# Kernel tuning notes

Measured on AMD Instinct MI355X. Metric: run time of the kernel, lower is better.

Reference implementation:

```python
import jax, jax.numpy as jnp
import numpy as np

B, T, D, H = 64, 512, 512, 512


def _gru_direction(x, w_ih, w_hh, b_ih, b_hh, reverse):
    # x: (B,T,D); w_ih: (3H,D); w_hh: (3H,H); biases: (3H,)
    # Precompute input projections for all timesteps (same math as per-step W_ih @ x_t).
    zi_all = jnp.einsum('btd,gd->btg', x, w_ih) + b_ih  # (B,T,3H)
    if reverse:
        zi_all = zi_all[:, ::-1]
    h0 = jnp.zeros((B, H), x.dtype)

    def step(h, zi):
        zh = h @ w_hh.T + b_hh                      # (B,3H), includes b_hh inside r-gated term
        r = jax.nn.sigmoid(zi[:, :H] + zh[:, :H])
        z = jax.nn.sigmoid(zi[:, H:2 * H] + zh[:, H:2 * H])
        n = jnp.tanh(zi[:, 2 * H:] + r * zh[:, 2 * H:])
        h_new = (1 - z) * n + z * h
        return h_new, h_new

    h_last, outs = jax.lax.scan(step, h0, jnp.swapaxes(zi_all, 0, 1))  # outs: (T,B,H)
    outs = jnp.swapaxes(outs, 0, 1)  # (B,T,H)
    if reverse:
        outs = outs[:, ::-1]
    return outs, h_last


def setup_inputs() -> dict:
    key = jax.random.key(0)
    ks = jax.random.split(key, 9)
    K = 1.0 / np.sqrt(H)

    def u(k, shape):
        return jax.random.uniform(k, shape, jnp.float32, -K, K)

    return {
        'x': jax.random.normal(ks[0], (B, T, D), jnp.float32),
        'w_ih_fw': u(ks[1], (3 * H, D)),
        'w_hh_fw': u(ks[2], (3 * H, H)),
        'b_ih_fw': u(ks[3], (3 * H,)),
        'b_hh_fw': u(ks[4], (3 * H,)),
        'w_ih_bw': u(ks[5], (3 * H, D)),
        'w_hh_bw': u(ks[6], (3 * H, H)),
        'b_ih_bw': u(ks[7], (3 * H,)),
        'b_hh_bw': u(ks[8], (3 * H,)),
    }


def reference(x, w_ih_fw, w_hh_fw, b_ih_fw, b_hh_fw, w_ih_bw, w_hh_bw, b_ih_bw, b_hh_bw):
    out_fw, h_fw = _gru_direction(x, w_ih_fw, w_hh_fw, b_ih_fw, b_hh_fw, reverse=False)
    out_bw, h_bw = _gru_direction(x, w_ih_bw, w_hh_bw, b_ih_bw, b_hh_bw, reverse=True)
    outputs = jnp.concatenate([out_fw, out_bw], axis=2)  # (B,T,2H)
    return outputs, h_fw, h_bw
```

## Files before the change

### kernel.cpp

```cpp
#include <hip/hip_runtime.h>
#include <hip/hip_bf16.h>

typedef __bf16 bf16_t;
typedef bf16_t bf16x8 __attribute__((ext_vector_type(8)));
typedef float  f32x4  __attribute__((ext_vector_type(4)));

constexpr int Bb = 64;
constexpr int T  = 512;
constexpr int D  = 512;
constexpr int H  = 512;
constexpr int M1 = Bb * T;
constexpr int N1 = 3 * H;

#define LDK 72

template <typename ZT>
__global__ __launch_bounds__(256) void zi_gemm(
    const float* __restrict__ x,
    const float* __restrict__ w_fw, const float* __restrict__ w_bw,
    const float* __restrict__ b_fw, const float* __restrict__ b_bw,
    ZT* __restrict__ zi)
{
    const int dir = blockIdx.z;
    const float* __restrict__ w    = dir ? w_bw : w_fw;
    const float* __restrict__ bias = dir ? b_bw : b_fw;
    ZT* __restrict__ out = zi + (size_t)dir * M1 * N1;

    const int m0 = blockIdx.x * 128;
    const int n0 = blockIdx.y * 128;

    __shared__ bf16_t As[128 * LDK];
    __shared__ bf16_t Bs[128 * LDK];

    const int tid  = threadIdx.x;
    const int lane = tid & 63;
    const int wave = tid >> 6;
    const int wm = (wave >> 1) * 64;
    const int wn = (wave & 1) * 64;
    const int q   = lane >> 4;
    const int l16 = lane & 15;

    f32x4 acc[4][4] = {};

    for (int kt = 0; kt < D; kt += 64) {
#pragma unroll
        for (int p = 0; p < 4; ++p) {
            int idx = tid + p * 256;
            int row = idx >> 3;
            int seg = idx & 7;
            const float* sa = &x[(size_t)(m0 + row) * D + kt + seg * 8];
            const float* sb = &w[(size_t)(n0 + row) * D + kt + seg * 8];
            float4 a0 = *(const float4*)sa;
            float4 a1 = *(const float4*)(sa + 4);
            float4 b0 = *(const float4*)sb;
            float4 b1 = *(const float4*)(sb + 4);
            bf16x8 ta = { (bf16_t)a0.x, (bf16_t)a0.y, (bf16_t)a0.z, (bf16_t)a0.w,
                          (bf16_t)a1.x, (bf16_t)a1.y, (bf16_t)a1.z, (bf16_t)a1.w };
            bf16x8 tb = { (bf16_t)b0.x, (bf16_t)b0.y, (bf16_t)b0.z, (bf16_t)b0.w,
                          (bf16_t)b1.x, (bf16_t)b1.y, (bf16_t)b1.z, (bf16_t)b1.w };
            *(bf16x8*)&As[row * LDK + seg * 8] = ta;
            *(bf16x8*)&Bs[row * LDK + seg * 8] = tb;
        }
        __syncthreads();
#pragma unroll
        for (int kk = 0; kk < 64; kk += 32) {
            bf16x8 afr[4], bfr[4];
#pragma unroll
            for (int i = 0; i < 4; ++i)
                afr[i] = *(const bf16x8*)&As[(wm + i * 16 + l16) * LDK + kk + q * 8];
#pragma unroll
            for (int j = 0; j < 4; ++j)
                bfr[j] = *(const bf16x8*)&Bs[(wn + j * 16 + l16) * LDK + kk + q * 8];
#pragma unroll
            for (int i = 0; i < 4; ++i)
#pragma unroll
                for (int j = 0; j < 4; ++j)
                    acc[i][j] = __builtin_amdgcn_mfma_f32_16x16x32_bf16(
                        afr[i], bfr[j], acc[i][j], 0, 0, 0);
        }
        __syncthreads();
    }

#pragma unroll
    for (int i = 0; i < 4; ++i) {
        int grow = m0 + wm + i * 16 + q * 4;
#pragma unroll
        for (int j = 0; j < 4; ++j) {
            int gcol = n0 + wn + j * 16 + l16;
            float bia = bias[gcol];
#pragma unroll
            for (int r = 0; r < 4; ++r) {
                float v = acc[i][j][r] + bia;
                out[(size_t)(grow + r) * N1 + gcol] = (ZT)v;
            }
        }
    }
}

template <typename ZT>
__device__ __forceinline__ float zcvt(unsigned v)
{
    if constexpr (sizeof(ZT) == 4)
        return __builtin_bit_cast(float, v);
    else
        return __builtin_bit_cast(float, v << 16);
}

template <typename ZT>
__global__ __launch_bounds__(256, 1) void gru_persist(
    const ZT* __restrict__ zi,
    const float* __restrict__ whh_fw,
    const float* __restrict__ whh_bw,
    const float* __restrict__ bhh_fw,
    const float* __restrict__ bhh_bw,
    bf16_t* __restrict__ hb16,
    float* __restrict__ out,
    float* __restrict__ hlast,
    unsigned int* __restrict__ bar)
{
    const int dir = blockIdx.y;
    const float* __restrict__ whh = dir ? whh_bw : whh_fw;
    const float* __restrict__ bhh = dir ? bhh_bw : bhh_fw;
    const ZT* __restrict__ zid = zi + (size_t)dir * M1 * N1;
    unsigned int* cnt = bar + dir * 32;

    const int tid  = threadIdx.x;
    const int lane = tid & 63;
    const int wave = tid >> 6;
    const int q    = lane >> 4;
    const int l16  = lane & 15;
    const int c0   = blockIdx.x * 16;
    const int wm   = wave * 16;
    const int c    = c0 + l16;

    bf16x8 wreg[3][16];
#pragma unroll
    for (int g = 0; g < 3; ++g) {
        const float* wr = &whh[(size_t)(g * H + c0 + l16) * H];
#pragma unroll
        for (int kt = 0; kt < 16; ++kt) {
            float4 a = *(const float4*)&wr[kt * 32 + q * 8];
            float4 b = *(const float4*)&wr[kt * 32 + q * 8 + 4];
            wreg[g][kt] = (bf16x8){ (bf16_t)a.x, (bf16_t)a.y, (bf16_t)a.z, (bf16_t)a.w,
                                    (bf16_t)b.x, (bf16_t)b.y, (bf16_t)b.z, (bf16_t)b.w };
        }
    }
    const float bh_r = bhh[c];
    const float bh_z = bhh[H + c];
    const float bh_n = bhh[2 * H + c];

    bf16_t* hbase16 = hb16 + (size_t)dir * 2 * Bb * H;
    const bf16_t* rd0 = hbase16 + (size_t)(wm + l16) * H + q * 8;
    const bf16_t* rd1 = rd0 + Bb * H;
    bf16_t* wr0 = hbase16 + (size_t)(wm + q * 4) * H + c;
    bf16_t* wr1 = wr0 + Bb * H;

    float hcur[4] = {0.f, 0.f, 0.f, 0.f};

    unsigned zr[3][4];

#define ISSUE_ZI(tt) do {                                                         \
    _Pragma("unroll")                                                             \
    for (int r_ = 0; r_ < 4; ++r_) {                                              \
        const ZT* zb_ = zid + ((size_t)(wm + q * 4 + r_) * T + (size_t)(tt)) * N1 \
                            + H + c;                                              \
        if constexpr (sizeof(ZT) == 4) {                                          \
            asm volatile("global_load_dword %0, %1, off offset:-2048"             \
                         : "=&v"(zr[0][r_]) : "v"(zb_) : "memory");               \
            asm volatile("global_load_dword %0, %1, off"                          \
                         : "=&v"(zr[1][r_]) : "v"(zb_) : "memory");               \
            asm volatile("global_load_dword %0, %1, off offset:2048"              \
                         : "=&v"(zr[2][r_]) : "v"(zb_) : "memory");               \
        } else {                                                                  \
            asm volatile("global_load_ushort %0, %1, off offset:-1024"            \
                         : "=&v"(zr[0][r_]) : "v"(zb_) : "memory");               \
            asm volatile("global_load_ushort %0, %1, off"                         \
                         : "=&v"(zr[1][r_]) : "v"(zb_) : "memory");               \
            asm volatile("global_load_ushort %0, %1, off offset:1024"             \
                         : "=&v"(zr[2][r_]) : "v"(zb_) : "memory");               \
        }                                                                         \
    }                                                                             \
} while (0)

    {
        const int t0 = dir ? (T - 1) : 0;
        ISSUE_ZI(t0);
    }

#pragma unroll 1
    for (int s = 0; s < T; ++s) {
        const int t = dir ? (T - 1 - s) : s;
        const bf16_t* hrd = (s & 1) ? rd1 : rd0;
        bf16_t*       hwr = (s & 1) ? wr0 : wr1;

        bf16x8 hf[16];
#define LDH(i, OFFSTR)                                                        \
        asm volatile("global_load_dwordx4 %0, %1, off offset:" OFFSTR         \
                     " sc0 sc1" : "=&v"(hf[i]) : "v"(hrd) : "memory");
        LDH(0,  "0")    LDH(1,  "64")   LDH(2,  "128")  LDH(3,  "192")
        LDH(4,  "256")  LDH(5,  "320")  LDH(6,  "384")  LDH(7,  "448")
        LDH(8,  "512")  LDH(9,  "576")  LDH(10, "640")  LDH(11, "704")
        LDH(12, "768")  LDH(13, "832")  LDH(14, "896")  LDH(15, "960")
#undef LDH
        __builtin_amdgcn_sched_barrier(0);
        asm volatile("s_waitcnt vmcnt(0)" ::: "memory");
        __builtin_amdgcn_sched_barrier(0);

        f32x4 acc[3][2] = {};
#pragma unroll
        for (int kt = 0; kt < 16; ++kt) {
#pragma unroll
            for (int g = 0; g < 3; ++g)
                acc[g][kt & 1] = __builtin_amdgcn_mfma_f32_16x16x32_bf16(
                    hf[kt], wreg[g][kt], acc[g][kt & 1], 0, 0, 0);
        }

        float hn4[4];
#pragma unroll
        for (int r = 0; r < 4; ++r) {
            float zh_r = acc[0][0][r] + acc[0][1][r] + bh_r;
            float zh_z = acc[1][0][r] + acc[1][1][r] + bh_z;
            float zh_n = acc[2][0][r] + acc[2][1][r] + bh_n;
            float zi_r = zcvt<ZT>(zr[0][r]);
            float zi_z = zcvt<ZT>(zr[1][r]);
            float zi_n = zcvt<ZT>(zr[2][r]);
            float rg = 1.f / (1.f + __expf(-(zi_r + zh_r)));
            float zg = 1.f / (1.f + __expf(-(zi_z + zh_z)));
            float ng = tanhf(zi_n + rg * zh_n);
            float hn = (1.f - zg) * ng + zg * hcur[r];
            hcur[r] = hn;
            hn4[r] = hn;
        }

        __builtin_amdgcn_sched_barrier(0);
#pragma unroll
        for (int r = 0; r < 4; ++r) {
            const int row = wm + q * 4 + r;
            unsigned short hs = __builtin_bit_cast(unsigned short, (bf16_t)hn4[r]);
            asm volatile("global_store_short %0, %1, off sc0 sc1"
                         :: "v"(hwr + (size_t)r * H), "v"(hs) : "memory");
            float* optr = out + ((size_t)row * T + t) * (2 * H) + (size_t)dir * H + c;
            asm volatile("global_store_dword %0, %1, off"
                         :: "v"(optr), "v"(hn4[r]) : "memory");
        }
        __builtin_amdgcn_sched_barrier(0);

        if (s < T - 1) {
            const int tn = dir ? (T - 2 - s) : (s + 1);
            ISSUE_ZI(tn);
            __builtin_amdgcn_sched_barrier(0);
            asm volatile("s_waitcnt vmcnt(12)" ::: "memory");
            __builtin_amdgcn_sched_barrier(0);
            __syncthreads();
            if (tid == 0) {
                __hip_atomic_fetch_add(cnt, 1u, __ATOMIC_RELAXED,
                                       __HIP_MEMORY_SCOPE_AGENT);
                const unsigned target = 32u * (unsigned)(s + 1);
                unsigned tries = 0;
                while (__hip_atomic_load(cnt, __ATOMIC_RELAXED,
                                         __HIP_MEMORY_SCOPE_AGENT) < target) {
                    __builtin_amdgcn_s_sleep(1);
                    if (++tries > 1000000u) break;
                }
            }
            __syncthreads();
        } else {
#pragma unroll
            for (int r = 0; r < 4; ++r) {
                const int row = wm + q * 4 + r;
                hlast[((size_t)dir * Bb + row) * H + c] = hn4[r];
            }
        }
    }
#undef ISSUE_ZI
}

extern "C" void kernel_launch(void* const* d_in, const int* in_sizes, int n_in,
                              void* d_out, int out_size, void* d_ws, size_t ws_size,
                              hipStream_t stream)
{
    const float* x       = (const float*)d_in[0];
    const float* w_ih_fw = (const float*)d_in[1];
    const float* w_hh_fw = (const float*)d_in[2];
    const float* b_ih_fw = (const float*)d_in[3];
    const float* b_hh_fw = (const float*)d_in[4];
    const float* w_ih_bw = (const float*)d_in[5];
    const float* w_hh_bw = (const float*)d_in[6];
    const float* b_ih_bw = (const float*)d_in[7];
    const float* b_hh_bw = (const float*)d_in[8];

    float* out   = (float*)d_out;
    float* hlast = out + (size_t)Bb * T * 2 * H;

    char* ws = (char*)d_ws;
    bf16_t*       hb16 = (bf16_t*)ws;
    unsigned int* bar  = (unsigned int*)(ws + 262144);
    void*         zi   = (void*)(ws + (1u << 20));

    const size_t need_f32 = (1ull << 20) + 2ull * M1 * N1 * sizeof(float);
    const bool use_f32 = (ws_size >= need_f32);

    hipMemsetAsync(d_ws, 0, 262144 + 256, stream);

    dim3 g1(M1 / 128, N1 / 128, 2);
    dim3 g2(32, 2);

    if (use_f32) {
        float* zif = (float*)zi;
        zi_gemm<float><<<g1, 256, 0, stream>>>(
            x, w_ih_fw, w_ih_bw, b_ih_fw, b_ih_bw, zif);
        gru_persist<float><<<g2, 256, 0, stream>>>(
            (const float*)zif, w_hh_fw, w_hh_bw, b_hh_fw, b_hh_bw,
            hb16, out, hlast, bar);
    } else {
        bf16_t* zib = (bf16_t*)zi;
        zi_gemm<bf16_t><<<g1, 256, 0, stream>>>(
            x, w_ih_fw, w_ih_bw, b_ih_fw, b_ih_bw, zib);
        gru_persist<bf16_t><<<g2, 256, 0, stream>>>(
            (const bf16_t*)zib, w_hh_fw, w_hh_bw, b_hh_fw, b_hh_bw,
            hb16, out, hlast, bar);
    }
}
```

Measured before the change: 3.073 ms.

## Replace block atomic barrier with per-wave flag barrier in GRU recurrence

```diff
diff --git a/kernel.cpp b/kernel.cpp
--- a/kernel.cpp
+++ b/kernel.cpp
@@ -122,7 +122,7 @@
     const float* __restrict__ whh = dir ? whh_bw : whh_fw;
     const float* __restrict__ bhh = dir ? bhh_bw : bhh_fw;
     const ZT* __restrict__ zid = zi + (size_t)dir * M1 * N1;
-    unsigned int* cnt = bar + dir * 32;
+    unsigned int* flags = bar + dir * 128;
 
     const int tid  = threadIdx.x;
     const int lane = tid & 63;
@@ -132,6 +132,7 @@
     const int c0   = blockIdx.x * 16;
     const int wm   = wave * 16;
     const int c    = c0 + l16;
+    const int gwave = blockIdx.x * 4 + wave;
 
     bf16x8 wreg[3][16];
 #pragma unroll
@@ -235,39 +236,55 @@
         __builtin_amdgcn_sched_barrier(0);
 #pragma unroll
         for (int r = 0; r < 4; ++r) {
-            const int row = wm + q * 4 + r;
             unsigned short hs = __builtin_bit_cast(unsigned short, (bf16_t)hn4[r]);
             asm volatile("global_store_short %0, %1, off sc0 sc1"
                          :: "v"(hwr + (size_t)r * H), "v"(hs) : "memory");
-            float* optr = out + ((size_t)row * T + t) * (2 * H) + (size_t)dir * H + c;
-            asm volatile("global_store_dword %0, %1, off"
-                         :: "v"(optr), "v"(hn4[r]) : "memory");
-        }
+        }
+        __builtin_amdgcn_sched_barrier(0);
+        asm volatile("s_waitcnt vmcnt(0)" ::: "memory");
         __builtin_amdgcn_sched_barrier(0);
 
         if (s < T - 1) {
+            if (lane == 0) {
+                unsigned fv = (unsigned)(s + 1);
+                asm volatile("global_store_dword %0, %1, off sc0 sc1"
+                             :: "v"(flags + gwave), "v"(fv) : "memory");
+            }
             const int tn = dir ? (T - 2 - s) : (s + 1);
             ISSUE_ZI(tn);
+#pragma unroll
+            for (int r = 0; r < 4; ++r) {
+                const int row = wm + q * 4 + r;
+                float* optr = out + ((size_t)row * T + t) * (2 * H)
+                                  + (size_t)dir * H + c;
+                asm volatile("global_store_dword %0, %1, off"
+                             :: "v"(optr), "v"(hn4[r]) : "memory");
+            }
             __builtin_amdgcn_sched_barrier(0);
-            asm volatile("s_waitcnt vmcnt(12)" ::: "memory");
-            __builtin_amdgcn_sched_barrier(0);
-            __syncthreads();
-            if (tid == 0) {
-                __hip_atomic_fetch_add(cnt, 1u, __ATOMIC_RELAXED,
-                                       __HIP_MEMORY_SCOPE_AGENT);
-                const unsigned target = 32u * (unsigned)(s + 1);
+            {
+                const unsigned tgt = (unsigned)(s + 1);
+                const unsigned int* f0 = flags + lane;
+                const unsigned int* f1 = flags + 64 + lane;
                 unsigned tries = 0;
-                while (__hip_atomic_load(cnt, __ATOMIC_RELAXED,
-                                         __HIP_MEMORY_SCOPE_AGENT) < target) {
+                for (;;) {
+                    unsigned a = __hip_atomic_load(f0, __ATOMIC_RELAXED,
+                                                   __HIP_MEMORY_SCOPE_AGENT);
+                    unsigned b = __hip_atomic_load(f1, __ATOMIC_RELAXED,
+                                                   __HIP_MEMORY_SCOPE_AGENT);
+                    if (__all(a >= tgt && b >= tgt)) break;
                     __builtin_amdgcn_s_sleep(1);
                     if (++tries > 1000000u) break;
                 }
             }
-            __syncthreads();
+            __builtin_amdgcn_sched_barrier(0);
         } else {
 #pragma unroll
             for (int r = 0; r < 4; ++r) {
                 const int row = wm + q * 4 + r;
+                float* optr = out + ((size_t)row * T + t) * (2 * H)
+                                  + (size_t)dir * H + c;
+                asm volatile("global_store_dword %0, %1, off"
+                             :: "v"(optr), "v"(hn4[r]) : "memory");
                 hlast[((size_t)dir * Bb + row) * H + c] = hn4[r];
             }
         }
@@ -300,7 +317,7 @@
     const size_t need_f32 = (1ull << 20) + 2ull * M1 * N1 * sizeof(float);
     const bool use_f32 = (ws_size >= need_f32);
 
-    hipMemsetAsync(d_ws, 0, 262144 + 256, stream);
+    hipMemsetAsync(d_ws, 0, 262144 + 1024, stream);
 
     dim3 g1(M1 / 128, N1 / 128, 2);
     dim3 g2(32, 2);
```

New measurement: 4.369 ms. +42.2%, slower.

## Split recurrent GRU into independent batch cliques with 4-block barriers

Applied to the files above, without the earlier changes.

```diff
diff --git a/kernel.cpp b/kernel.cpp
--- a/kernel.cpp
+++ b/kernel.cpp
@@ -107,7 +107,7 @@
 }
 
 template <typename ZT>
-__global__ __launch_bounds__(256, 1) void gru_persist(
+__global__ __launch_bounds__(512) void gru_persist(
     const ZT* __restrict__ zi,
     const float* __restrict__ whh_fw,
     const float* __restrict__ whh_bw,
@@ -116,27 +116,31 @@
     bf16_t* __restrict__ hb16,
     float* __restrict__ out,
     float* __restrict__ hlast,
-    unsigned int* __restrict__ bar)
+    unsigned int* __restrict__ ctrl)
 {
-    const int dir = blockIdx.y;
-    const float* __restrict__ whh = dir ? whh_bw : whh_fw;
-    const float* __restrict__ bhh = dir ? bhh_bw : bhh_fw;
-    const ZT* __restrict__ zid = zi + (size_t)dir * M1 * N1;
-    unsigned int* cnt = bar + dir * 32;
-
     const int tid  = threadIdx.x;
     const int lane = tid & 63;
     const int wave = tid >> 6;
     const int q    = lane >> 4;
     const int l16  = lane & 15;
-    const int c0   = blockIdx.x * 16;
-    const int wm   = wave * 16;
-    const int c    = c0 + l16;
+
+    const int clique = blockIdx.x & 7;
+    const int role   = blockIdx.x >> 3;
+    const int dir    = clique >> 2;
+    const int grp    = clique & 3;
+    const int cw     = role * 128 + wave * 16;
+    const int c      = cw + l16;
+    const int wmg    = grp * 16;
+
+    const float* __restrict__ whh = dir ? whh_bw : whh_fw;
+    const float* __restrict__ bhh = dir ? bhh_bw : bhh_fw;
+    const ZT* __restrict__ zid = zi + (size_t)dir * M1 * N1;
+    unsigned int* cnt = ctrl + clique * 64;
 
     bf16x8 wreg[3][16];
 #pragma unroll
     for (int g = 0; g < 3; ++g) {
-        const float* wr = &whh[(size_t)(g * H + c0 + l16) * H];
+        const float* wr = &whh[(size_t)(g * H + cw + l16) * H];
 #pragma unroll
         for (int kt = 0; kt < 16; ++kt) {
             float4 a = *(const float4*)&wr[kt * 32 + q * 8];
@@ -149,20 +153,19 @@
     const float bh_z = bhh[H + c];
     const float bh_n = bhh[2 * H + c];
 
-    bf16_t* hbase16 = hb16 + (size_t)dir * 2 * Bb * H;
-    const bf16_t* rd0 = hbase16 + (size_t)(wm + l16) * H + q * 8;
-    const bf16_t* rd1 = rd0 + Bb * H;
-    bf16_t* wr0 = hbase16 + (size_t)(wm + q * 4) * H + c;
-    bf16_t* wr1 = wr0 + Bb * H;
+    bf16_t* hc = hb16 + (size_t)clique * 2 * 16 * H;
+    const bf16_t* rd0 = hc + (size_t)l16 * H + q * 8;
+    const bf16_t* rd1 = rd0 + 16 * H;
+    bf16_t* wr0 = hc + (size_t)(q * 4) * H + c;
+    bf16_t* wr1 = wr0 + 16 * H;
 
     float hcur[4] = {0.f, 0.f, 0.f, 0.f};
-
     unsigned zr[3][4];
 
 #define ISSUE_ZI(tt) do {                                                         \
     _Pragma("unroll")                                                             \
     for (int r_ = 0; r_ < 4; ++r_) {                                              \
-        const ZT* zb_ = zid + ((size_t)(wm + q * 4 + r_) * T + (size_t)(tt)) * N1 \
+        const ZT* zb_ = zid + ((size_t)(wmg + q * 4 + r_) * T + (size_t)(tt)) * N1\
                             + H + c;                                              \
         if constexpr (sizeof(ZT) == 4) {                                          \
             asm volatile("global_load_dword %0, %1, off offset:-2048"             \
@@ -235,30 +238,34 @@
         __builtin_amdgcn_sched_barrier(0);
 #pragma unroll
         for (int r = 0; r < 4; ++r) {
-            const int row = wm + q * 4 + r;
             unsigned short hs = __builtin_bit_cast(unsigned short, (bf16_t)hn4[r]);
             asm volatile("global_store_short %0, %1, off sc0 sc1"
                          :: "v"(hwr + (size_t)r * H), "v"(hs) : "memory");
-            float* optr = out + ((size_t)row * T + t) * (2 * H) + (size_t)dir * H + c;
-            asm volatile("global_store_dword %0, %1, off"
-                         :: "v"(optr), "v"(hn4[r]) : "memory");
-        }
+        }
+        __builtin_amdgcn_sched_barrier(0);
+        asm volatile("s_waitcnt vmcnt(0)" ::: "memory");
         __builtin_amdgcn_sched_barrier(0);
 
         if (s < T - 1) {
             const int tn = dir ? (T - 2 - s) : (s + 1);
             ISSUE_ZI(tn);
-            __builtin_amdgcn_sched_barrier(0);
-            asm volatile("s_waitcnt vmcnt(12)" ::: "memory");
+#pragma unroll
+            for (int r = 0; r < 4; ++r) {
+                const int row = wmg + q * 4 + r;
+                float* optr = out + ((size_t)row * T + t) * (2 * H)
+                                  + (size_t)dir * H + c;
+                asm volatile("global_store_dword %0, %1, off"
+                             :: "v"(optr), "v"(hn4[r]) : "memory");
+            }
             __builtin_amdgcn_sched_barrier(0);
             __syncthreads();
             if (tid == 0) {
                 __hip_atomic_fetch_add(cnt, 1u, __ATOMIC_RELAXED,
                                        __HIP_MEMORY_SCOPE_AGENT);
-                const unsigned target = 32u * (unsigned)(s + 1);
+                const unsigned tgt = 4u * (unsigned)(s + 1);
                 unsigned tries = 0;
                 while (__hip_atomic_load(cnt, __ATOMIC_RELAXED,
-                                         __HIP_MEMORY_SCOPE_AGENT) < target) {
+                                         __HIP_MEMORY_SCOPE_AGENT) < tgt) {
                     __builtin_amdgcn_s_sleep(1);
                     if (++tries > 1000000u) break;
                 }
@@ -267,7 +274,11 @@
         } else {
 #pragma unroll
             for (int r = 0; r < 4; ++r) {
-                const int row = wm + q * 4 + r;
+                const int row = wmg + q * 4 + r;
+                float* optr = out + ((size_t)row * T + t) * (2 * H)
+                                  + (size_t)dir * H + c;
+                asm volatile("global_store_dword %0, %1, off"
+                             :: "v"(optr), "v"(hn4[r]) : "memory");
                 hlast[((size_t)dir * Bb + row) * H + c] = hn4[r];
             }
         }
@@ -294,30 +305,30 @@
 
     char* ws = (char*)d_ws;
     bf16_t*       hb16 = (bf16_t*)ws;
-    unsigned int* bar  = (unsigned int*)(ws + 262144);
+    unsigned int* ctrl = (unsigned int*)(ws + 262144);
     void*         zi   = (void*)(ws + (1u << 20));
 
     const size_t need_f32 = (1ull << 20) + 2ull * M1 * N1 * sizeof(float);
     const bool use_f32 = (ws_size >= need_f32);
 
-    hipMemsetAsync(d_ws, 0, 262144 + 256, stream);
+    hipMemsetAsync(d_ws, 0, 262144 + 2048, stream);
 
     dim3 g1(M1 / 128, N1 / 128, 2);
-    dim3 g2(32, 2);
+    dim3 g2(32);
 
     if (use_f32) {
         float* zif = (float*)zi;
         zi_gemm<float><<<g1, 256, 0, stream>>>(
             x, w_ih_fw, w_ih_bw, b_ih_fw, b_ih_bw, zif);
-        gru_persist<float><<<g2, 256, 0, stream>>>(
+        gru_persist<float><<<g2, 512, 0, stream>>>(
             (const float*)zif, w_hh_fw, w_hh_bw, b_hh_fw, b_hh_bw,
-            hb16, out, hlast, bar);
+            hb16, out, hlast, ctrl);
     } else {
         bf16_t* zib = (bf16_t*)zi;
         zi_gemm<bf16_t><<<g1, 256, 0, stream>>>(
             x, w_ih_fw, w_ih_bw, b_ih_fw, b_ih_bw, zib);
-        gru_persist<bf16_t><<<g2, 256, 0, stream>>>(
+        gru_persist<bf16_t><<<g2, 512, 0, stream>>>(
             (const bf16_t*)zib, w_hh_fw, w_hh_bw, b_hh_fw, b_hh_bw,
-            hb16, out, hlast, bar);
+            hb16, out, hlast, ctrl);
     }
 }
```

Measured after the change: 6.283 ms. 104% more time.
